# Kernel optimization log

Measured on AMD Instinct MI355X. Metric: run time of the kernel, lower is better.

The kernel has to match this reference:

```python
import jax, jax.numpy as jnp
import numpy as np

B = 262144
HIST = 24
FORE = 20
HID = 256
# torch: tau_int = clamp(tau,1,18).long().item(); default tau=6.0 -> static 6 (host sync in torch)
TAU_INT = 6


def setup_inputs() -> dict:
    key = jax.random.key(0)
    ks = jax.random.split(key, 9)
    s = 0.1
    return {
        "history": jax.random.normal(ks[0], (B, HIST), jnp.float32),
        "enc_w1": jax.random.normal(ks[1], (HIST + FORE, HID), jnp.float32) * s,
        "enc_b1": jnp.zeros((HID,), jnp.float32),
        "enc_w2": jax.random.normal(ks[2], (HID, HID), jnp.float32) * s,
        "enc_b2": jnp.zeros((HID,), jnp.float32),
        "cor_w1": jax.random.normal(ks[3], (HID, HID), jnp.float32) * s,
        "cor_b1": jnp.zeros((HID,), jnp.float32),
        "cor_w2": jax.random.normal(ks[4], (HID, FORE), jnp.float32) * s,
        "cor_b2": jnp.zeros((FORE,), jnp.float32),
        "alpha": jnp.float32(0.2),
        "beta": jnp.float32(0.3),
        "gamma": jnp.float32(0.01),
        "tau": jnp.float32(6.0),
        "lambda_mix": jnp.float32(0.5),
    }


def _physics_core(history, alpha, beta, gamma, steps):
    a = jax.nn.sigmoid(alpha)
    b = jax.nn.sigmoid(beta)
    g = jnp.abs(gamma)
    T0 = history[:, -1]                      # [B]
    buf0 = history[:, -TAU_INT:].T           # [tau, B]; buf0[0] = history[:, -tau]

    def step(carry, _):
        T, buf = carry
        T_delayed = buf[0]
        T_new = T - a * T - b * T_delayed - g * T ** 3
        buf = jnp.concatenate([buf[1:], T_new[None, :]], axis=0)
        return (T_new, buf), T_new

    _, preds = jax.lax.scan(step, (T0, buf0), None, length=steps)
    return preds.T                            # [B, steps]


def reference(history, enc_w1, enc_b1, enc_w2, enc_b2,
              cor_w1, cor_b1, cor_w2, cor_b2,
              alpha, beta, gamma, tau, lambda_mix):
    T_physics = _physics_core(history, alpha, beta, gamma, FORE)   # [B, FORE]
    combined = jnp.concatenate([history, T_physics], axis=1)       # [B, HIST+FORE]
    h = jnp.tanh(combined @ enc_w1 + enc_b1)
    features = jnp.tanh(h @ enc_w2 + enc_b2)
    c = jnp.tanh(features @ cor_w1 + cor_b1)
    T_soft = c @ cor_w2 + cor_b2                                   # [B, FORE]
    lam = jax.nn.sigmoid(lambda_mix)
    T_pred = T_physics + lam * T_soft
    return (T_pred, T_physics, T_soft)
```

## Files before the change

### kernel.cpp

```cpp
#include <hip/hip_runtime.h>
#include <hip/hip_bf16.h>

#define NROWS 262144
#define HISTC 24
#define FOREC 20

typedef __bf16        v8bf __attribute__((ext_vector_type(8)));
typedef float         v4f  __attribute__((ext_vector_type(4)));
typedef float         v2f  __attribute__((ext_vector_type(2)));
typedef unsigned int  v4u  __attribute__((ext_vector_type(4)));
typedef unsigned int  v2u  __attribute__((ext_vector_type(2)));

#define WS_WT1_OFF 64
#define WT1_ELEMS 16384
#define WT2_ELEMS 65536
#define WT3_ELEMS 65536
#define WT4R_ELEMS 65536

#define TANH_C 2.885390081777927f

__device__ __forceinline__ unsigned short f2bf(float x) {
    unsigned u = __builtin_bit_cast(unsigned, x);
    u += 0x7FFFu + ((u >> 16) & 1u);
    return (unsigned short)(u >> 16);
}

__device__ __forceinline__ unsigned packbf2(float a, float b) {
    unsigned ua = __builtin_bit_cast(unsigned, a) + 0x8000u;
    unsigned ub = __builtin_bit_cast(unsigned, b) + 0x8000u;
    return __builtin_amdgcn_perm(ub, ua, 0x07060302u);
}

__device__ __forceinline__ void lds_barrier() {
    asm volatile("s_waitcnt lgkmcnt(0)\n\ts_barrier" ::: "memory");
}

__global__ void prep_kernel(const float* __restrict__ w1, const float* __restrict__ w2,
                            const float* __restrict__ w3, const float* __restrict__ w4,
                            const float* __restrict__ alpha, const float* __restrict__ beta,
                            const float* __restrict__ gamma, const float* __restrict__ lmix,
                            unsigned char* __restrict__ ws)
{
    if (blockIdx.x == 104) {
        int t = threadIdx.x;
        float* wsf = (float*)ws;
        if (t == 0) wsf[0] = 1.0f / (1.0f + expf(-alpha[0]));
        else if (t == 1) wsf[1] = 1.0f / (1.0f + expf(-beta[0]));
        else if (t == 2) wsf[2] = fabsf(gamma[0]);
        else if (t == 3) wsf[3] = 1.0f / (1.0f + expf(-lmix[0]));
        return;
    }
    int idx = (blockIdx.x * 256 + threadIdx.x) * 8;
    const float* src;
    int KT, Kreal, Nreal, srcN, local, ntmask;
    unsigned short* dst = (unsigned short*)(ws + WS_WT1_OFF);
    if (idx < WT1_ELEMS) {
        local = idx; src = w1; KT = 2; Kreal = 44; Nreal = 256; srcN = 256; ntmask = 255;
    } else if (idx < WT1_ELEMS + WT2_ELEMS) {
        local = idx - WT1_ELEMS; dst += WT1_ELEMS;
        src = w2; KT = 8; Kreal = 256; Nreal = 256; srcN = 256; ntmask = 255;
    } else if (idx < WT1_ELEMS + WT2_ELEMS + WT3_ELEMS) {
        local = idx - (WT1_ELEMS + WT2_ELEMS); dst += WT1_ELEMS + WT2_ELEMS;
        src = w3; KT = 8; Kreal = 256; Nreal = 256; srcN = 256; ntmask = 255;
    } else {
        local = idx - (WT1_ELEMS + WT2_ELEMS + WT3_ELEMS);
        dst += WT1_ELEMS + WT2_ELEMS + WT3_ELEMS;
        src = w4; KT = 8; Kreal = 256; Nreal = 20; srcN = 20; ntmask = 1;
    }
    int L   = (local >> 3) & 63;
    int blk = local >> 9;
    int kt = blk % KT, nt = (blk / KT) & ntmask;
    int cc = L & 15,  qq = L >> 4;
    int feat = nt * 16 + cc;
    int kbase = kt * 32 + qq * 8;
    unsigned short tmp[8];
#pragma unroll
    for (int j = 0; j < 8; ++j) {
        int k = kbase + j;
        float v = (k < Kreal && feat < Nreal) ? src[k * srcN + feat] : 0.0f;
        tmp[j] = f2bf(v);
    }
    v4u pk;
    pk[0] = tmp[0] | ((unsigned)tmp[1] << 16);
    pk[1] = tmp[2] | ((unsigned)tmp[3] << 16);
    pk[2] = tmp[4] | ((unsigned)tmp[5] << 16);
    pk[3] = tmp[6] | ((unsigned)tmp[7] << 16);
    *(v4u*)&dst[local] = pk;
}

template<int KT, int KTN, int S0>
__device__ __forceinline__ void layer_pipe(unsigned short* buf,
        const v4u* __restrict__ wp, const v4u* __restrict__ wpn,
        const float* __restrict__ bias, v4u A[3][4],
        int w, int c, int q, int lane)
{
    v4f acc[4][4];
#pragma unroll
    for (int ft = 0; ft < 4; ++ft)
#pragma unroll
        for (int st = 0; st < 4; ++st) {
            v4f z = {0.0f, 0.0f, 0.0f, 0.0f};
            acc[ft][st] = z;
        }

#pragma unroll
    for (int kt = 0; kt < KT; ++kt) {
        const int cs = (S0 + kt) % 3;
        const int ps = (S0 + kt + 2) % 3;
        if (kt + 2 < KT) {
#pragma unroll
            for (int ft = 0; ft < 4; ++ft)
                A[ps][ft] = wp[((w * 4 + ft) * KT + kt + 2) * 64 + lane];
        } else {
#pragma unroll
            for (int ft = 0; ft < 4; ++ft)
                A[ps][ft] = wpn[((w * 4 + ft) * KTN + (kt + 2 - KT)) * 64 + lane];
        }
#pragma unroll
        for (int st = 0; st < 4; ++st) {
            v4u braw = *(const v4u*)&buf[(st * 16 + c) * 264 + kt * 32 + q * 8];
            v8bf bb = __builtin_bit_cast(v8bf, braw);
#pragma unroll
            for (int ft = 0; ft < 4; ++ft)
                acc[ft][st] = __builtin_amdgcn_mfma_f32_16x16x32_bf16(
                    __builtin_bit_cast(v8bf, A[cs][ft]), bb, acc[ft][st], 0, 0, 0);
        }
    }

    lds_barrier();

#pragma unroll
    for (int ft = 0; ft < 4; ++ft) {
        v4f bi = *(const v4f*)&bias[w * 64 + ft * 16 + q * 4];
        v4f bic;
#pragma unroll
        for (int r = 0; r < 4; ++r) bic[r] = bi[r] * TANH_C;
#pragma unroll
        for (int st = 0; st < 4; ++st) {
            float x[4];
#pragma unroll
            for (int r = 0; r < 4; ++r) {
                float t = __builtin_fmaf(acc[ft][st][r], TANH_C, bic[r]);
                float p = __builtin_amdgcn_exp2f(t);
                float rc = __builtin_amdgcn_rcpf(p + 1.0f);
                x[r] = __builtin_fmaf(-2.0f, rc, 1.0f);
            }
            v2u d; d[0] = packbf2(x[0], x[1]); d[1] = packbf2(x[2], x[3]);
            *(v2u*)&buf[(st * 16 + c) * 264 + w * 64 + ft * 16 + q * 4] = d;
        }
    }
    lds_barrier();
}

__global__ __launch_bounds__(256, 3) void fused_kernel(
    const float* __restrict__ history,
    const float* __restrict__ eb1, const float* __restrict__ eb2,
    const float* __restrict__ cb1, const float* __restrict__ cb2,
    const unsigned char* __restrict__ ws, float* __restrict__ out)
{
    __shared__ unsigned short buf[64 * 264];
    __shared__ float tp[64 * 20];

    const int tid  = threadIdx.x;
    const int w    = tid >> 6;
    const int lane = tid & 63;
    const int c    = lane & 15;
    const int q    = lane >> 4;
    const int row0 = blockIdx.x << 6;
    const float* wsf = (const float*)ws;
    const v4u* wp1 = (const v4u*)(ws + WS_WT1_OFF);
    const v4u* wp2 = wp1 + WT1_ELEMS / 8;
    const v4u* wp3 = wp2 + WT2_ELEMS / 8;
    const v4u* wp4 = wp3 + WT3_ELEMS / 8;

    v4u A[3][4];
#pragma unroll
    for (int ft = 0; ft < 4; ++ft) {
        A[0][ft] = wp1[((w * 4 + ft) * 2 + 0) * 64 + lane];
        A[1][ft] = wp1[((w * 4 + ft) * 2 + 1) * 64 + lane];
    }

#pragma unroll
    for (int i = 0; i < 2; ++i) {
        int e = tid + i * 256;
        if (e < 384) {
            int r  = e / 6, c4 = e - r * 6;
            v4f h4 = *(const v4f*)&history[(long)(row0 + r) * 24 + c4 * 4];
            v2u d; d[0] = packbf2(h4[0], h4[1]); d[1] = packbf2(h4[2], h4[3]);
            *(v2u*)&buf[r * 264 + c4 * 4] = d;
        }
    }
#pragma unroll
    for (int i = 0; i < 2; ++i) {
        int e = tid + i * 256;
        if (e < 320) {
            int r = e / 5, g = e - r * 5;
            v2u z = {0u, 0u};
            *(v2u*)&buf[r * 264 + 44 + g * 4] = z;
        }
    }
    if (tid < 64) {
        const float* hrow = &history[(long)(row0 + tid) * 24];
        v2f h18 = *(const v2f*)&hrow[18];
        v4f h20 = *(const v4f*)&hrow[20];
        float pa = wsf[0], pb = wsf[1], pg = wsf[2];
        float d0 = h18[0], d1 = h18[1], d2 = h20[0];
        float d3 = h20[1], d4 = h20[2], d5 = h20[3];
        float T = d5;
#pragma unroll
        for (int s = 0; s < 20; ++s) {
            float t3 = T * T * T;
            float Tn = T - pa * T;
            Tn = Tn - pb * d0;
            Tn = Tn - pg * t3;
            tp[tid * 20 + s] = Tn;
            buf[tid * 264 + 24 + s] = f2bf(Tn);
            d0 = d1; d1 = d2; d2 = d3; d3 = d4; d4 = d5; d5 = Tn;
            T = Tn;
        }
    }
    lds_barrier();

    layer_pipe<2, 8, 0>(buf, wp1, wp2, eb1, A, w, c, q, lane);
    layer_pipe<8, 8, 2>(buf, wp2, wp3, eb2, A, w, c, q, lane);
    layer_pipe<8, 8, 1>(buf, wp3, wp4, cb1, A, w, c, q, lane);

    v4f acc40 = {0.0f, 0.0f, 0.0f, 0.0f}, acc41 = {0.0f, 0.0f, 0.0f, 0.0f};
#pragma unroll
    for (int kt = 0; kt < 8; ++kt) {
        const int cs = kt % 3, ps = (kt + 2) % 3;
        if (kt + 2 < 8) {
            A[ps][0] = wp4[((w * 4 + 0) * 8 + kt + 2) * 64 + lane];
            A[ps][1] = wp4[((w * 4 + 1) * 8 + kt + 2) * 64 + lane];
        }
        v4u braw = *(const v4u*)&buf[(w * 16 + c) * 264 + kt * 32 + q * 8];
        v8bf bb = __builtin_bit_cast(v8bf, braw);
        acc40 = __builtin_amdgcn_mfma_f32_16x16x32_bf16(
            __builtin_bit_cast(v8bf, A[cs][0]), bb, acc40, 0, 0, 0);
        acc41 = __builtin_amdgcn_mfma_f32_16x16x32_bf16(
            __builtin_bit_cast(v8bf, A[cs][1]), bb, acc41, 0, 0, 0);
    }

    const float lam = wsf[3];
    const long sample = (long)row0 + w * 16 + c;
    float* outP = out;
    float* outF = out + (long)NROWS * 20;
    float* outS = out + (long)NROWS * 40;
    {
        int f0 = q * 4;
        v4f bi  = *(const v4f*)&cb2[f0];
        v4f tph = *(const v4f*)&tp[(w * 16 + c) * 20 + f0];
        v4f ts, pr;
#pragma unroll
        for (int r = 0; r < 4; ++r) {
            ts[r] = acc40[r] + bi[r];
            pr[r] = tph[r] + lam * ts[r];
        }
        *(v4f*)&outS[sample * 20 + f0] = ts;
        *(v4f*)&outP[sample * 20 + f0] = pr;
        *(v4f*)&outF[sample * 20 + f0] = tph;
    }
    if (q == 0) {
        v4f bi  = *(const v4f*)&cb2[16];
        v4f tph = *(const v4f*)&tp[(w * 16 + c) * 20 + 16];
        v4f ts, pr;
#pragma unroll
        for (int r = 0; r < 4; ++r) {
            ts[r] = acc41[r] + bi[r];
            pr[r] = tph[r] + lam * ts[r];
        }
        *(v4f*)&outS[sample * 20 + 16] = ts;
        *(v4f*)&outP[sample * 20 + 16] = pr;
        *(v4f*)&outF[sample * 20 + 16] = tph;
    }
}

extern "C" void kernel_launch(void* const* d_in, const int* in_sizes, int n_in,
                              void* d_out, int out_size, void* d_ws, size_t ws_size,
                              hipStream_t stream)
{
    const float* history = (const float*)d_in[0];
    const float* enc_w1  = (const float*)d_in[1];
    const float* enc_b1  = (const float*)d_in[2];
    const float* enc_w2  = (const float*)d_in[3];
    const float* enc_b2  = (const float*)d_in[4];
    const float* cor_w1  = (const float*)d_in[5];
    const float* cor_b1  = (const float*)d_in[6];
    const float* cor_w2  = (const float*)d_in[7];
    const float* cor_b2  = (const float*)d_in[8];
    const float* alpha   = (const float*)d_in[9];
    const float* beta    = (const float*)d_in[10];
    const float* gamma   = (const float*)d_in[11];
    const float* lmix    = (const float*)d_in[13];

    prep_kernel<<<105, 256, 0, stream>>>(enc_w1, enc_w2, cor_w1, cor_w2,
                                         alpha, beta, gamma, lmix,
                                         (unsigned char*)d_ws);
    fused_kernel<<<NROWS / 64, 256, 0, stream>>>(history, enc_b1, enc_b2, cor_b1, cor_b2,
                                                 (const unsigned char*)d_ws, (float*)d_out);
}
```

Before: 204.1 us.

## Swizzle LDS activation buffer, drop physics LDS tile, raise occupancy

```diff
diff --git a/kernel.cpp b/kernel.cpp
--- a/kernel.cpp
+++ b/kernel.cpp
@@ -33,6 +33,10 @@
 
 __device__ __forceinline__ void lds_barrier() {
     asm volatile("s_waitcnt lgkmcnt(0)\n\ts_barrier" ::: "memory");
+}
+
+__device__ __forceinline__ int swzi(int r, int byteoff) {
+    return (r << 8) + (((byteoff) ^ ((r & 7) << 4)) >> 1);
 }
 
 __global__ void prep_kernel(const float* __restrict__ w1, const float* __restrict__ w2,
@@ -118,7 +122,7 @@
         }
 #pragma unroll
         for (int st = 0; st < 4; ++st) {
-            v4u braw = *(const v4u*)&buf[(st * 16 + c) * 264 + kt * 32 + q * 8];
+            v4u braw = *(const v4u*)&buf[swzi(st * 16 + c, kt * 64 + q * 16)];
             v8bf bb = __builtin_bit_cast(v8bf, braw);
 #pragma unroll
             for (int ft = 0; ft < 4; ++ft)
@@ -146,20 +150,19 @@
                 x[r] = __builtin_fmaf(-2.0f, rc, 1.0f);
             }
             v2u d; d[0] = packbf2(x[0], x[1]); d[1] = packbf2(x[2], x[3]);
-            *(v2u*)&buf[(st * 16 + c) * 264 + w * 64 + ft * 16 + q * 4] = d;
+            *(v2u*)&buf[swzi(st * 16 + c, w * 128 + ft * 32 + q * 8)] = d;
         }
     }
     lds_barrier();
 }
 
-__global__ __launch_bounds__(256, 3) void fused_kernel(
+__global__ __launch_bounds__(256, 5) void fused_kernel(
     const float* __restrict__ history,
     const float* __restrict__ eb1, const float* __restrict__ eb2,
     const float* __restrict__ cb1, const float* __restrict__ cb2,
     const unsigned char* __restrict__ ws, float* __restrict__ out)
 {
-    __shared__ unsigned short buf[64 * 264];
-    __shared__ float tp[64 * 20];
+    __shared__ unsigned short buf[64 * 256];
 
     const int tid  = threadIdx.x;
     const int w    = tid >> 6;
@@ -187,7 +190,7 @@
             int r  = e / 6, c4 = e - r * 6;
             v4f h4 = *(const v4f*)&history[(long)(row0 + r) * 24 + c4 * 4];
             v2u d; d[0] = packbf2(h4[0], h4[1]); d[1] = packbf2(h4[2], h4[3]);
-            *(v2u*)&buf[r * 264 + c4 * 4] = d;
+            *(v2u*)&buf[swzi(r, c4 * 8)] = d;
         }
     }
 #pragma unroll
@@ -196,7 +199,7 @@
         if (e < 320) {
             int r = e / 5, g = e - r * 5;
             v2u z = {0u, 0u};
-            *(v2u*)&buf[r * 264 + 44 + g * 4] = z;
+            *(v2u*)&buf[swzi(r, 88 + g * 8)] = z;
         }
     }
     if (tid < 64) {
@@ -207,23 +210,37 @@
         float d0 = h18[0], d1 = h18[1], d2 = h20[0];
         float d3 = h20[1], d4 = h20[2], d5 = h20[3];
         float T = d5;
+        float pr[20];
 #pragma unroll
         for (int s = 0; s < 20; ++s) {
             float t3 = T * T * T;
             float Tn = T - pa * T;
             Tn = Tn - pb * d0;
             Tn = Tn - pg * t3;
-            tp[tid * 20 + s] = Tn;
-            buf[tid * 264 + 24 + s] = f2bf(Tn);
+            pr[s] = Tn;
+            buf[swzi(tid, 48 + 2 * s)] = f2bf(Tn);
             d0 = d1; d1 = d2; d2 = d3; d3 = d4; d4 = d5; d5 = Tn;
             T = Tn;
         }
+        float* outF = out + (long)NROWS * 20;
+        const long samp = (long)row0 + tid;
+#pragma unroll
+        for (int g = 0; g < 5; ++g) {
+            v4f v = {pr[g * 4], pr[g * 4 + 1], pr[g * 4 + 2], pr[g * 4 + 3]};
+            *(v4f*)&outF[samp * 20 + g * 4] = v;
+        }
+        asm volatile("s_waitcnt vmcnt(0)" ::: "memory");
     }
     lds_barrier();
 
     layer_pipe<2, 8, 0>(buf, wp1, wp2, eb1, A, w, c, q, lane);
     layer_pipe<8, 8, 2>(buf, wp2, wp3, eb2, A, w, c, q, lane);
     layer_pipe<8, 8, 1>(buf, wp3, wp4, cb1, A, w, c, q, lane);
+
+    const long sample = (long)row0 + w * 16 + c;
+    const float* outFr = out + (long)NROWS * 20;
+    v4f tph0 = *(const v4f*)&outFr[sample * 20 + q * 4];
+    v4f tph1 = *(const v4f*)&outFr[sample * 20 + 16];
 
     v4f acc40 = {0.0f, 0.0f, 0.0f, 0.0f}, acc41 = {0.0f, 0.0f, 0.0f, 0.0f};
 #pragma unroll
@@ -233,7 +250,7 @@
             A[ps][0] = wp4[((w * 4 + 0) * 8 + kt + 2) * 64 + lane];
             A[ps][1] = wp4[((w * 4 + 1) * 8 + kt + 2) * 64 + lane];
         }
-        v4u braw = *(const v4u*)&buf[(w * 16 + c) * 264 + kt * 32 + q * 8];
+        v4u braw = *(const v4u*)&buf[swzi(w * 16 + c, kt * 64 + q * 16)];
         v8bf bb = __builtin_bit_cast(v8bf, braw);
         acc40 = __builtin_amdgcn_mfma_f32_16x16x32_bf16(
             __builtin_bit_cast(v8bf, A[cs][0]), bb, acc40, 0, 0, 0);
@@ -242,36 +259,30 @@
     }
 
     const float lam = wsf[3];
-    const long sample = (long)row0 + w * 16 + c;
     float* outP = out;
-    float* outF = out + (long)NROWS * 20;
     float* outS = out + (long)NROWS * 40;
     {
         int f0 = q * 4;
         v4f bi  = *(const v4f*)&cb2[f0];
-        v4f tph = *(const v4f*)&tp[(w * 16 + c) * 20 + f0];
-        v4f ts, pr;
+        v4f ts, prv;
 #pragma unroll
         for (int r = 0; r < 4; ++r) {
-            ts[r] = acc40[r] + bi[r];
-            pr[r] = tph[r] + lam * ts[r];
+            ts[r]  = acc40[r] + bi[r];
+            prv[r] = tph0[r] + lam * ts[r];
         }
         *(v4f*)&outS[sample * 20 + f0] = ts;
-        *(v4f*)&outP[sample * 20 + f0] = pr;
-        *(v4f*)&outF[sample * 20 + f0] = tph;
+        *(v4f*)&outP[sample * 20 + f0] = prv;
     }
     if (q == 0) {
         v4f bi  = *(const v4f*)&cb2[16];
-        v4f tph = *(const v4f*)&tp[(w * 16 + c) * 20 + 16];
-        v4f ts, pr;
+        v4f ts, prv;
 #pragma unroll
         for (int r = 0; r < 4; ++r) {
-            ts[r] = acc41[r] + bi[r];
-            pr[r] = tph[r] + lam * ts[r];
+            ts[r]  = acc41[r] + bi[r];
+            prv[r] = tph1[r] + lam * ts[r];
         }
         *(v4f*)&outS[sample * 20 + 16] = ts;
-        *(v4f*)&outP[sample * 20 + 16] = pr;
-        *(v4f*)&outF[sample * 20 + 16] = tph;
+        *(v4f*)&outP[sample * 20 + 16] = prv;
     }
 }
 
```

Measured after the change: 435.2 us. 2.13x slower.

## Swizzle LDS activations, shrink weight prefetch to double buffer, raise occupancy

Applied to the files above, without the earlier changes.

```diff
diff --git a/kernel.cpp b/kernel.cpp
--- a/kernel.cpp
+++ b/kernel.cpp
@@ -33,6 +33,10 @@
 
 __device__ __forceinline__ void lds_barrier() {
     asm volatile("s_waitcnt lgkmcnt(0)\n\ts_barrier" ::: "memory");
+}
+
+__device__ __forceinline__ int swzi(int r, int byteoff) {
+    return (r << 8) + (((byteoff) ^ ((r & 7) << 4)) >> 1);
 }
 
 __global__ void prep_kernel(const float* __restrict__ w1, const float* __restrict__ w2,
@@ -88,10 +92,10 @@
     *(v4u*)&dst[local] = pk;
 }
 
-template<int KT, int KTN, int S0>
+template<int KT, int KTN>
 __device__ __forceinline__ void layer_pipe(unsigned short* buf,
         const v4u* __restrict__ wp, const v4u* __restrict__ wpn,
-        const float* __restrict__ bias, v4u A[3][4],
+        const float* __restrict__ bias, v4u A[2][4],
         int w, int c, int q, int lane)
 {
     v4f acc[4][4];
@@ -105,20 +109,20 @@
 
 #pragma unroll
     for (int kt = 0; kt < KT; ++kt) {
-        const int cs = (S0 + kt) % 3;
-        const int ps = (S0 + kt + 2) % 3;
-        if (kt + 2 < KT) {
+        const int cs = kt & 1;
+        const int ps = cs ^ 1;
+        if (kt + 1 < KT) {
 #pragma unroll
             for (int ft = 0; ft < 4; ++ft)
-                A[ps][ft] = wp[((w * 4 + ft) * KT + kt + 2) * 64 + lane];
+                A[ps][ft] = wp[((w * 4 + ft) * KT + kt + 1) * 64 + lane];
         } else {
 #pragma unroll
             for (int ft = 0; ft < 4; ++ft)
-                A[ps][ft] = wpn[((w * 4 + ft) * KTN + (kt + 2 - KT)) * 64 + lane];
+                A[ps][ft] = wpn[((w * 4 + ft) * KTN + 0) * 64 + lane];
         }
 #pragma unroll
         for (int st = 0; st < 4; ++st) {
-            v4u braw = *(const v4u*)&buf[(st * 16 + c) * 264 + kt * 32 + q * 8];
+            v4u braw = *(const v4u*)&buf[swzi(st * 16 + c, kt * 64 + q * 16)];
             v8bf bb = __builtin_bit_cast(v8bf, braw);
 #pragma unroll
             for (int ft = 0; ft < 4; ++ft)
@@ -146,19 +150,19 @@
                 x[r] = __builtin_fmaf(-2.0f, rc, 1.0f);
             }
             v2u d; d[0] = packbf2(x[0], x[1]); d[1] = packbf2(x[2], x[3]);
-            *(v2u*)&buf[(st * 16 + c) * 264 + w * 64 + ft * 16 + q * 4] = d;
+            *(v2u*)&buf[swzi(st * 16 + c, w * 128 + ft * 32 + q * 8)] = d;
         }
     }
     lds_barrier();
 }
 
-__global__ __launch_bounds__(256, 3) void fused_kernel(
+__global__ __launch_bounds__(256, 4) void fused_kernel(
     const float* __restrict__ history,
     const float* __restrict__ eb1, const float* __restrict__ eb2,
     const float* __restrict__ cb1, const float* __restrict__ cb2,
     const unsigned char* __restrict__ ws, float* __restrict__ out)
 {
-    __shared__ unsigned short buf[64 * 264];
+    __shared__ unsigned short buf[64 * 256];
     __shared__ float tp[64 * 20];
 
     const int tid  = threadIdx.x;
@@ -173,12 +177,10 @@
     const v4u* wp3 = wp2 + WT2_ELEMS / 8;
     const v4u* wp4 = wp3 + WT3_ELEMS / 8;
 
-    v4u A[3][4];
-#pragma unroll
-    for (int ft = 0; ft < 4; ++ft) {
+    v4u A[2][4];
+#pragma unroll
+    for (int ft = 0; ft < 4; ++ft)
         A[0][ft] = wp1[((w * 4 + ft) * 2 + 0) * 64 + lane];
-        A[1][ft] = wp1[((w * 4 + ft) * 2 + 1) * 64 + lane];
-    }
 
 #pragma unroll
     for (int i = 0; i < 2; ++i) {
@@ -187,7 +189,7 @@
             int r  = e / 6, c4 = e - r * 6;
             v4f h4 = *(const v4f*)&history[(long)(row0 + r) * 24 + c4 * 4];
             v2u d; d[0] = packbf2(h4[0], h4[1]); d[1] = packbf2(h4[2], h4[3]);
-            *(v2u*)&buf[r * 264 + c4 * 4] = d;
+            *(v2u*)&buf[swzi(r, c4 * 8)] = d;
         }
     }
 #pragma unroll
@@ -196,7 +198,7 @@
         if (e < 320) {
             int r = e / 5, g = e - r * 5;
             v2u z = {0u, 0u};
-            *(v2u*)&buf[r * 264 + 44 + g * 4] = z;
+            *(v2u*)&buf[swzi(r, 88 + g * 8)] = z;
         }
     }
     if (tid < 64) {
@@ -214,26 +216,26 @@
             Tn = Tn - pb * d0;
             Tn = Tn - pg * t3;
             tp[tid * 20 + s] = Tn;
-            buf[tid * 264 + 24 + s] = f2bf(Tn);
+            buf[swzi(tid, 48 + 2 * s)] = f2bf(Tn);
             d0 = d1; d1 = d2; d2 = d3; d3 = d4; d4 = d5; d5 = Tn;
             T = Tn;
         }
     }
     lds_barrier();
 
-    layer_pipe<2, 8, 0>(buf, wp1, wp2, eb1, A, w, c, q, lane);
-    layer_pipe<8, 8, 2>(buf, wp2, wp3, eb2, A, w, c, q, lane);
-    layer_pipe<8, 8, 1>(buf, wp3, wp4, cb1, A, w, c, q, lane);
+    layer_pipe<2, 8>(buf, wp1, wp2, eb1, A, w, c, q, lane);
+    layer_pipe<8, 8>(buf, wp2, wp3, eb2, A, w, c, q, lane);
+    layer_pipe<8, 8>(buf, wp3, wp4, cb1, A, w, c, q, lane);
 
     v4f acc40 = {0.0f, 0.0f, 0.0f, 0.0f}, acc41 = {0.0f, 0.0f, 0.0f, 0.0f};
 #pragma unroll
     for (int kt = 0; kt < 8; ++kt) {
-        const int cs = kt % 3, ps = (kt + 2) % 3;
-        if (kt + 2 < 8) {
-            A[ps][0] = wp4[((w * 4 + 0) * 8 + kt + 2) * 64 + lane];
-            A[ps][1] = wp4[((w * 4 + 1) * 8 + kt + 2) * 64 + lane];
-        }
-        v4u braw = *(const v4u*)&buf[(w * 16 + c) * 264 + kt * 32 + q * 8];
+        const int cs = kt & 1, ps = cs ^ 1;
+        if (kt + 1 < 8) {
+            A[ps][0] = wp4[((w * 4 + 0) * 8 + kt + 1) * 64 + lane];
+            A[ps][1] = wp4[((w * 4 + 1) * 8 + kt + 1) * 64 + lane];
+        }
+        v4u braw = *(const v4u*)&buf[swzi(w * 16 + c, kt * 64 + q * 16)];
         v8bf bb = __builtin_bit_cast(v8bf, braw);
         acc40 = __builtin_amdgcn_mfma_f32_16x16x32_bf16(
             __builtin_bit_cast(v8bf, A[cs][0]), bb, acc40, 0, 0, 0);
```

Result: no change. 201.7 us (-1.2%).

## Double-buffer activations in LDS with XOR swizzle and prefetch B fragments

Applied to the files above, without the earlier changes.

```diff
diff --git a/kernel.cpp b/kernel.cpp
--- a/kernel.cpp
+++ b/kernel.cpp
@@ -33,6 +33,10 @@
 
 __device__ __forceinline__ void lds_barrier() {
     asm volatile("s_waitcnt lgkmcnt(0)\n\ts_barrier" ::: "memory");
+}
+
+__device__ __forceinline__ int swzi(int r, int byteoff) {
+    return (r << 8) + (((byteoff) ^ ((r & 7) << 4)) >> 1);
 }
 
 __global__ void prep_kernel(const float* __restrict__ w1, const float* __restrict__ w2,
@@ -89,10 +93,11 @@
 }
 
 template<int KT, int KTN, int S0>
-__device__ __forceinline__ void layer_pipe(unsigned short* buf,
+__device__ __forceinline__ void layer_pipe(const char* bin, char* bout,
         const v4u* __restrict__ wp, const v4u* __restrict__ wpn,
         const float* __restrict__ bias, v4u A[3][4],
-        int w, int c, int q, int lane)
+        const int* be, const int* bo, const int* wb, const int* fx,
+        int w, int q, int lane)
 {
     v4f acc[4][4];
 #pragma unroll
@@ -102,6 +107,11 @@
             v4f z = {0.0f, 0.0f, 0.0f, 0.0f};
             acc[ft][st] = z;
         }
+
+    v4u Bf[2][4];
+#pragma unroll
+    for (int st = 0; st < 4; ++st)
+        Bf[0][st] = *(const v4u*)(bin + be[st]);
 
 #pragma unroll
     for (int kt = 0; kt < KT; ++kt) {
@@ -116,18 +126,24 @@
             for (int ft = 0; ft < 4; ++ft)
                 A[ps][ft] = wpn[((w * 4 + ft) * KTN + (kt + 2 - KT)) * 64 + lane];
         }
+        if (kt + 1 < KT) {
+            const int kn = kt + 1;
+#pragma unroll
+            for (int st = 0; st < 4; ++st)
+                Bf[kn & 1][st] = *(const v4u*)(bin + ((kn & 1) ? bo[st] : be[st]) + kn * 64);
+        }
+        __builtin_amdgcn_s_setprio(1);
 #pragma unroll
         for (int st = 0; st < 4; ++st) {
-            v4u braw = *(const v4u*)&buf[(st * 16 + c) * 264 + kt * 32 + q * 8];
-            v8bf bb = __builtin_bit_cast(v8bf, braw);
+            v8bf bb = __builtin_bit_cast(v8bf, Bf[kt & 1][st]);
 #pragma unroll
             for (int ft = 0; ft < 4; ++ft)
                 acc[ft][st] = __builtin_amdgcn_mfma_f32_16x16x32_bf16(
                     __builtin_bit_cast(v8bf, A[cs][ft]), bb, acc[ft][st], 0, 0, 0);
         }
-    }
-
-    lds_barrier();
+        __builtin_amdgcn_s_setprio(0);
+    }
+
 
 #pragma unroll
     for (int ft = 0; ft < 4; ++ft) {
@@ -146,20 +162,22 @@
                 x[r] = __builtin_fmaf(-2.0f, rc, 1.0f);
             }
             v2u d; d[0] = packbf2(x[0], x[1]); d[1] = packbf2(x[2], x[3]);
-            *(v2u*)&buf[(st * 16 + c) * 264 + w * 64 + ft * 16 + q * 4] = d;
+            *(v2u*)(bout + wb[st] + fx[ft]) = d;
         }
     }
     lds_barrier();
 }
 
-__global__ __launch_bounds__(256, 3) void fused_kernel(
+__global__ __launch_bounds__(256, 2) void fused_kernel(
     const float* __restrict__ history,
     const float* __restrict__ eb1, const float* __restrict__ eb2,
     const float* __restrict__ cb1, const float* __restrict__ cb2,
     const unsigned char* __restrict__ ws, float* __restrict__ out)
 {
-    __shared__ unsigned short buf[64 * 264];
+    __shared__ unsigned short buf[2][64 * 256];
     __shared__ float tp[64 * 20];
+    char* b0 = (char*)&buf[0][0];
+    char* b1 = (char*)&buf[1][0];
 
     const int tid  = threadIdx.x;
     const int w    = tid >> 6;
@@ -173,6 +191,21 @@
     const v4u* wp3 = wp2 + WT2_ELEMS / 8;
     const v4u* wp4 = wp3 + WT3_ELEMS / 8;
 
+    const int e    = (c >> 2) & 1;
+    const int d64  = e << 6;
+    const int qp_r = (q * 16) ^ ((c & 3) << 4);
+    int be[4], bo[4], wb[4], fx[4];
+#pragma unroll
+    for (int st = 0; st < 4; ++st) {
+        int br = (st * 16 + c) * 512 + qp_r;
+        be[st] = br + d64;
+        bo[st] = br - d64;
+        wb[st] = (st * 16 + c) * 512 + w * 128 + ((q * 8) ^ ((c & 1) << 4));
+    }
+#pragma unroll
+    for (int ft = 0; ft < 4; ++ft)
+        fx[ft] = (ft * 32) ^ (((c >> 1) & 3) << 5);
+
     v4u A[3][4];
 #pragma unroll
     for (int ft = 0; ft < 4; ++ft) {
@@ -182,21 +215,21 @@
 
 #pragma unroll
     for (int i = 0; i < 2; ++i) {
-        int e = tid + i * 256;
-        if (e < 384) {
-            int r  = e / 6, c4 = e - r * 6;
+        int e2 = tid + i * 256;
+        if (e2 < 384) {
+            int r  = e2 / 6, c4 = e2 - r * 6;
             v4f h4 = *(const v4f*)&history[(long)(row0 + r) * 24 + c4 * 4];
             v2u d; d[0] = packbf2(h4[0], h4[1]); d[1] = packbf2(h4[2], h4[3]);
-            *(v2u*)&buf[r * 264 + c4 * 4] = d;
+            *(v2u*)&buf[0][swzi(r, c4 * 8)] = d;
         }
     }
 #pragma unroll
     for (int i = 0; i < 2; ++i) {
-        int e = tid + i * 256;
-        if (e < 320) {
-            int r = e / 5, g = e - r * 5;
+        int e2 = tid + i * 256;
+        if (e2 < 320) {
+            int r = e2 / 5, g = e2 - r * 5;
             v2u z = {0u, 0u};
-            *(v2u*)&buf[r * 264 + 44 + g * 4] = z;
+            *(v2u*)&buf[0][swzi(r, 88 + g * 8)] = z;
         }
     }
     if (tid < 64) {
@@ -214,18 +247,20 @@
             Tn = Tn - pb * d0;
             Tn = Tn - pg * t3;
             tp[tid * 20 + s] = Tn;
-            buf[tid * 264 + 24 + s] = f2bf(Tn);
+            buf[0][swzi(tid, 48 + 2 * s)] = f2bf(Tn);
             d0 = d1; d1 = d2; d2 = d3; d3 = d4; d4 = d5; d5 = Tn;
             T = Tn;
         }
     }
     lds_barrier();
 
-    layer_pipe<2, 8, 0>(buf, wp1, wp2, eb1, A, w, c, q, lane);
-    layer_pipe<8, 8, 2>(buf, wp2, wp3, eb2, A, w, c, q, lane);
-    layer_pipe<8, 8, 1>(buf, wp3, wp4, cb1, A, w, c, q, lane);
-
+    layer_pipe<2, 8, 0>(b0, b1, wp1, wp2, eb1, A, be, bo, wb, fx, w, q, lane);
+    layer_pipe<8, 8, 2>(b1, b0, wp2, wp3, eb2, A, be, bo, wb, fx, w, q, lane);
+    layer_pipe<8, 8, 1>(b0, b1, wp3, wp4, cb1, A, be, bo, wb, fx, w, q, lane);
+
+    const int b04 = (w * 16 + c) * 512 + qp_r;
     v4f acc40 = {0.0f, 0.0f, 0.0f, 0.0f}, acc41 = {0.0f, 0.0f, 0.0f, 0.0f};
+    v4u bcur = *(const v4u*)(b1 + b04 + d64);
 #pragma unroll
     for (int kt = 0; kt < 8; ++kt) {
         const int cs = kt % 3, ps = (kt + 2) % 3;
@@ -233,12 +268,14 @@
             A[ps][0] = wp4[((w * 4 + 0) * 8 + kt + 2) * 64 + lane];
             A[ps][1] = wp4[((w * 4 + 1) * 8 + kt + 2) * 64 + lane];
         }
-        v4u braw = *(const v4u*)&buf[(w * 16 + c) * 264 + kt * 32 + q * 8];
-        v8bf bb = __builtin_bit_cast(v8bf, braw);
+        v4u bnext;
+        if (kt + 1 < 8)
+            bnext = *(const v4u*)(b1 + b04 + (((kt + 1) & 1) ? -d64 : d64) + (kt + 1) * 64);
         acc40 = __builtin_amdgcn_mfma_f32_16x16x32_bf16(
-            __builtin_bit_cast(v8bf, A[cs][0]), bb, acc40, 0, 0, 0);
+            __builtin_bit_cast(v8bf, A[cs][0]), __builtin_bit_cast(v8bf, bcur), acc40, 0, 0, 0);
         acc41 = __builtin_amdgcn_mfma_f32_16x16x32_bf16(
-            __builtin_bit_cast(v8bf, A[cs][1]), bb, acc41, 0, 0, 0);
+            __builtin_bit_cast(v8bf, A[cs][1]), __builtin_bit_cast(v8bf, bcur), acc41, 0, 0, 0);
+        if (kt + 1 < 8) bcur = bnext;
     }
 
     const float lam = wsf[3];
```

New measurement: 200.4 us. No clear change (-1.8%).
